# Kernel optimization log

Measured on AMD Instinct MI355X. Metric: run time of the kernel, lower is better.

The kernel has to match this reference:

```python
import jax, jax.numpy as jnp
import numpy as np

Q = 128


def _maxpool2(x):
    # 2x2 max pool, stride 2, NCHW
    return jax.lax.reduce_window(x, -jnp.inf, jax.lax.max,
                                 (1, 1, 2, 2), (1, 1, 2, 2), 'VALID')


def _conv(x, w, b):
    y = jax.lax.conv_general_dilated(x, w, window_strides=(1, 1), padding='VALID',
                                     dimension_numbers=('NCHW', 'OIHW', 'NCHW'))
    return y + b[None, :, None, None]


def setup_inputs() -> dict:
    key = jax.random.key(0)
    ks = jax.random.split(key, 16)
    B = 4096
    x = jax.random.normal(ks[0], (B, 1, 28, 28), dtype=jnp.float32)
    hash_idx1 = jax.random.randint(ks[1], (25,), 0, Q, dtype=jnp.int32)
    hash_idx2 = jax.random.randint(ks[2], (800,), 0, Q, dtype=jnp.int32)
    hash_idx3 = jax.random.randint(ks[3], (1024,), 0, Q, dtype=jnp.int32)
    # random +/-1 signs
    sgn1 = jnp.sign(jax.random.normal(ks[4], (25,), dtype=jnp.float32))
    sgn2 = jnp.sign(jax.random.normal(ks[5], (800,), dtype=jnp.float32))
    sgn3 = jnp.sign(jax.random.normal(ks[6], (1024,), dtype=jnp.float32))
    # compressed (sketched) parameters: one length-Q vector per output unit
    w1 = jax.random.normal(ks[7], (32, Q), dtype=jnp.float32) * 0.2
    b1 = jax.random.normal(ks[8], (32,), dtype=jnp.float32) * 0.05
    w2 = jax.random.normal(ks[9], (64, Q), dtype=jnp.float32) * 0.05
    b2 = jax.random.normal(ks[10], (64,), dtype=jnp.float32) * 0.05
    w3 = jax.random.normal(ks[11], (512, Q), dtype=jnp.float32) * 0.03
    b3 = jax.random.normal(ks[12], (512,), dtype=jnp.float32) * 0.05
    fc2_w = jax.random.normal(ks[13], (10, 512), dtype=jnp.float32) * 0.04
    fc2_b = jax.random.normal(ks[14], (10,), dtype=jnp.float32) * 0.05
    return {'x': x,
            'hash_idx1': hash_idx1, 'hash_idx2': hash_idx2, 'hash_idx3': hash_idx3,
            'sgn1': sgn1, 'sgn2': sgn2, 'sgn3': sgn3,
            'w1': w1, 'b1': b1, 'w2': w2, 'b2': b2, 'w3': w3, 'b3': b3,
            'fc2_w': fc2_w, 'fc2_b': fc2_b}


def reference(x, hash_idx1, hash_idx2, hash_idx3, sgn1, sgn2, sgn3,
              w1, b1, w2, b2, w3, b3, fc2_w, fc2_b):
    # SketchConv1: reconstruct dense weight via gather + sign flip
    wc1 = (w1[:, hash_idx1] * sgn1[None, :]).reshape(32, 1, 5, 5)
    h = jax.nn.relu(_maxpool2(_conv(x, wc1, b1)))          # (B,32,12,12)
    # SketchConv2
    wc2 = (w2[:, hash_idx2] * sgn2[None, :]).reshape(64, 32, 5, 5)
    h = jax.nn.relu(_maxpool2(_conv(h, wc2, b2)))          # (B,64,4,4)
    h = h.reshape(h.shape[0], -1)                          # (B,1024)
    # SketchLinear
    W3 = w3[:, hash_idx3] * sgn3[None, :]                  # (512,1024)
    h = jax.nn.relu(h @ W3.T + b3)                         # (B,512)
    logits = h @ fc2_w.T + fc2_b                           # (B,10)
    return jax.nn.log_softmax(logits, axis=1)
```

## Files before the change

### kernel.cpp

```cpp
#include <hip/hip_runtime.h>
#include <hip/hip_bf16.h>
#include <math.h>


typedef __attribute__((ext_vector_type(8))) short bf16x8;
typedef __attribute__((ext_vector_type(4))) float f32x4;

static __device__ inline ushort f2bfu(float v) {
    union { __hip_bfloat16 h; ushort u; } cv;
    cv.h = __float2bfloat16(v);
    return cv.u;
}


__global__ __launch_bounds__(256)
void k_reconstruct(const float* __restrict__ w1, const float* __restrict__ w2,
                   const float* __restrict__ w3,
                   const int* __restrict__ hi1, const int* __restrict__ hi2,
                   const int* __restrict__ hi3,
                   const float* __restrict__ s1, const float* __restrict__ s2,
                   const float* __restrict__ s3,
                   __hip_bfloat16* __restrict__ wc1f,
                   __hip_bfloat16* __restrict__ wc1s,
                   __hip_bfloat16* __restrict__ wc2f,
                   __hip_bfloat16* __restrict__ W3f) {
    const int t = blockIdx.x * blockDim.x + threadIdx.x;
    bf16x8 o;
    if (t < 256) {
        const bool shifted = t >= 128;
        const int u = t & 127;
        const int nt = u >> 6, lane = u & 63;
        const int quad = lane >> 4, l15 = lane & 15;
        const int oc = nt * 16 + l15;
        #pragma unroll
        for (int j = 0; j < 8; ++j) {
            int tt = quad * 8 + j;
            int ki = (tt * 43) >> 8;
            int kj = tt - 6 * ki;
            float v = 0.f;
            if (!shifted && ki < 5 && kj < 5) {
                int f = ki * 5 + kj;
                v = w1[oc * 128 + hi1[f]] * s1[f];
            } else if (shifted && ki < 5 && kj >= 1 && kj <= 5) {
                int f = ki * 5 + (kj - 1);
                v = w1[oc * 128 + hi1[f]] * s1[f];
            }
            o[j] = (short)f2bfu(v);
        }
        *(bf16x8*)((ushort*)(shifted ? wc1s : wc1f) + (size_t)u * 8) = o;
    } else if (t < 6656) {
        const int u = t - 256;
        const int l15 = u & 15, quad = (u >> 4) & 3;
        const int ntA = (u >> 6) & 3, tap = u >> 8;
        const int oc = ntA * 16 + l15;
        #pragma unroll
        for (int j = 0; j < 8; ++j) {
            int ic = quad * 8 + j;
            int f = ic * 25 + tap;
            o[j] = (short)f2bfu(w2[oc * 128 + hi2[f]] * s2[f]);
        }
        *(bf16x8*)((ushort*)wc2f + (size_t)u * 8) = o;
    } else if (t < 72192) {
        const int u = t - 6656;
        const int l15 = u & 15, quad = (u >> 4) & 3;
        const int kt = (u >> 6) & 31, ntile = u >> 11;
        const int n = ntile * 16 + l15;
        #pragma unroll
        for (int j = 0; j < 8; ++j) {
            int k = kt * 32 + quad * 8 + j;
            o[j] = (short)f2bfu(w3[n * 128 + hi3[k]] * s3[k]);
        }
        *(bf16x8*)((ushort*)W3f + (size_t)u * 8) = o;
    }
}

__global__ __launch_bounds__(512, 6)
void k_conv(const float* __restrict__ x,
            const __hip_bfloat16* __restrict__ wc1f,
            const __hip_bfloat16* __restrict__ wc1s,
            const __hip_bfloat16* __restrict__ wc2f,
            const float* __restrict__ b1, const float* __restrict__ b2,
            __hip_bfloat16* __restrict__ h2) {
    __shared__ __align__(16) ushort s_xb[4 * 816];
    __shared__ __align__(16) ushort s_h1[16 * 1160];

    const int tid = threadIdx.x;
    const int b0 = blockIdx.x * 4;
    const int wave = tid >> 6, lane = tid & 63;
    const int l15 = lane & 15, quad = lane >> 4;

    {
        const float4* xg = (const float4*)(x + (size_t)b0 * 784);
        for (int i = tid; i < 784; i += 512) {
            float4 v = xg[i];
            int img = i / 196;
            int pos = (i - img * 196) * 4;
            ushort* dst = &s_xb[img * 816 + pos];
            dst[0] = f2bfu(v.x); dst[1] = f2bfu(v.y);
            dst[2] = f2bfu(v.z); dst[3] = f2bfu(v.w);
        }
        if (tid < 128) {
            int img = tid >> 5, k = tid & 31;
            s_xb[img * 816 + 784 + k] = 0;
        }
    }

    bf16x8 bw1[2], bw1s[2];
    float bb1[2];
    #pragma unroll
    for (int nt = 0; nt < 2; ++nt) {
        bw1[nt]  = *(const bf16x8*)((const ushort*)wc1f + (nt * 64 + lane) * 8);
        bw1s[nt] = *(const bf16x8*)((const ushort*)wc1s + (nt * 64 + lane) * 8);
        bb1[nt] = b1[nt * 16 + l15];
    }
    __syncthreads();

    {
        const int img = wave >> 1, half = wave & 1;
        const int sub = l15 & 3;
        const ushort* srcImg = s_xb + img * 816;
        int offr[4];
        #pragma unroll
        for (int r = 0; r < 4; ++r) {
            int t = quad * 8 + 2 * r;
            int row = (t * 43) >> 8;
            int col = t - 6 * row;
            offr[r] = row * 28 + col;
        }
        const int g0 = l15 >> 3, r0 = l15 & 7;
        #pragma unroll
        for (int ii = 0; ii < 18; ++ii) {
            const int i = half * 18 + ii;
            const int pb = 4 * i + (l15 >> 2);
            const int pi = (pb * 171) >> 11;
            const int pj = pb - 12 * pi;
            const int base_e = (2 * pi + (sub >> 1)) * 28 + 2 * pj;
            const ushort* p0 = srcImg + base_e;
            union { bf16x8 v; uint u[4]; } A;
            A.u[0] = *(const uint*)(p0 + offr[0]);
            A.u[1] = *(const uint*)(p0 + offr[1]);
            A.u[2] = *(const uint*)(p0 + offr[2]);
            A.u[3] = *(const uint*)(p0 + offr[3]);
            f32x4 z = {0.f, 0.f, 0.f, 0.f};
            f32x4 ce0 = __builtin_amdgcn_mfma_f32_16x16x32_bf16(A.v, bw1[0],  z, 0, 0, 0);
            f32x4 co0 = __builtin_amdgcn_mfma_f32_16x16x32_bf16(A.v, bw1s[0], z, 0, 0, 0);
            f32x4 ce1 = __builtin_amdgcn_mfma_f32_16x16x32_bf16(A.v, bw1[1],  z, 0, 0, 0);
            f32x4 co1 = __builtin_amdgcn_mfma_f32_16x16x32_bf16(A.v, bw1s[1], z, 0, 0, 0);
            const int pbo = 4 * i + quad;
            float m0 = fmaxf(fmaxf(ce0[0], co0[1]), fmaxf(ce0[2], co0[3]));
            float m1 = fmaxf(fmaxf(ce1[0], co1[1]), fmaxf(ce1[2], co1[3]));
            s_h1[(img * 4 + g0) * 1160 + pbo * 8 + r0]     = f2bfu(fmaxf(m0 + bb1[0], 0.f));
            s_h1[(img * 4 + 2 + g0) * 1160 + pbo * 8 + r0] = f2bfu(fmaxf(m1 + bb1[1], 0.f));
        }
    }
    __syncthreads();

    const int pr = wave >> 1, nh = wave & 1;
    const int sub2 = l15 & 3;
    const int ci2 = 2 * pr + (sub2 >> 1);
    const int cj2 = 2 * (l15 >> 2) + (sub2 & 1);
    const int posBase = (ci2 * 12 + cj2) * 8;

    f32x4 acc[4][2];
    float bb2[2];
    #pragma unroll
    for (int ntl = 0; ntl < 2; ++ntl) {
        bb2[ntl] = b2[(nh * 2 + ntl) * 16 + l15];
        #pragma unroll
        for (int img = 0; img < 4; ++img)
            acc[img][ntl] = (f32x4){0.f, 0.f, 0.f, 0.f};
    }

    #pragma unroll
    for (int tap = 0; tap < 25; ++tap) {
        const int ki = tap / 5, kj = tap % 5;
        const int off = (ki * 12 + kj) * 8;
        bf16x8 a[4];
        #pragma unroll
        for (int img = 0; img < 4; ++img)
            a[img] = *(const bf16x8*)&s_h1[(img * 4 + quad) * 1160 + posBase + off];
        #pragma unroll
        for (int ntl = 0; ntl < 2; ++ntl) {
            bf16x8 bf = *(const bf16x8*)((const ushort*)wc2f +
                          ((tap * 4 + nh * 2 + ntl) * 64 + lane) * 8);
            #pragma unroll
            for (int img = 0; img < 4; ++img)
                acc[img][ntl] = __builtin_amdgcn_mfma_f32_16x16x32_bf16(
                    a[img], bf, acc[img][ntl], 0, 0, 0);
        }
    }

    #pragma unroll
    for (int img = 0; img < 4; ++img)
        #pragma unroll
        for (int ntl = 0; ntl < 2; ++ntl) {
            f32x4 c = acc[img][ntl];
            float m = fmaxf(fmaxf(c[0], c[1]), fmaxf(c[2], c[3]));
            float v = fmaxf(m + bb2[ntl], 0.f);
            h2[(size_t)(b0 + img) * 1024 + ((nh * 2 + ntl) * 16 + l15) * 16 + pr * 4 + quad] =
                __float2bfloat16(v);
        }
}

__global__ __launch_bounds__(1024)
void k_fc(const __hip_bfloat16* __restrict__ A, const __hip_bfloat16* __restrict__ W3f,
          const float* __restrict__ b3, const float* __restrict__ fc2w,
          const float* __restrict__ fc2b, float* __restrict__ out) {
    __shared__ __align__(16) ushort s_A[16 * 1032];
    __shared__ float s_h3[16 * 516];

    const int tid = threadIdx.x;
    const int wave = tid >> 6, lane = tid & 63;
    const int l15 = lane & 15, quad = lane >> 4;
    const int mBase = blockIdx.x * 16;

    {
        const uint4* g = (const uint4*)(A + (size_t)(mBase + wave) * 1024);
        uint4 v0 = g[lane * 2], v1 = g[lane * 2 + 1];
        uint4* d = (uint4*)&s_A[wave * 1032 + lane * 16];
        d[0] = v0; d[1] = v1;
    }
    __syncthreads();

    f32x4 acc[2];
    acc[0] = (f32x4){0.f, 0.f, 0.f, 0.f};
    acc[1] = (f32x4){0.f, 0.f, 0.f, 0.f};

    const ushort* aP = &s_A[l15 * 1032 + quad * 8];
    const ushort* bP0 = (const ushort*)W3f + (((size_t)(wave * 2)     * 32) * 64 + lane) * 8;
    const ushort* bP1 = (const ushort*)W3f + (((size_t)(wave * 2 + 1) * 32) * 64 + lane) * 8;
    #pragma unroll 4
    for (int kt = 0; kt < 32; ++kt) {
        bf16x8 a = *(const bf16x8*)(aP + kt * 32);
        bf16x8 bf0 = *(const bf16x8*)(bP0 + kt * 512);
        bf16x8 bf1 = *(const bf16x8*)(bP1 + kt * 512);
        acc[0] = __builtin_amdgcn_mfma_f32_16x16x32_bf16(a, bf0, acc[0], 0, 0, 0);
        acc[1] = __builtin_amdgcn_mfma_f32_16x16x32_bf16(a, bf1, acc[1], 0, 0, 0);
    }

    #pragma unroll
    for (int ntl = 0; ntl < 2; ++ntl) {
        int col = wave * 32 + ntl * 16 + l15;
        float bb = b3[col];
        #pragma unroll
        for (int r = 0; r < 4; ++r)
            s_h3[(quad * 4 + r) * 516 + col] = fmaxf(acc[ntl][r] + bb, 0.f);
    }
    __syncthreads();

    const float* hrow = &s_h3[wave * 516];
    float4 h0 = *(const float4*)&hrow[lane * 8];
    float4 h1 = *(const float4*)&hrow[lane * 8 + 4];
    float lg[10];
    #pragma unroll
    for (int c = 0; c < 10; ++c) {
        float4 w0 = *(const float4*)&fc2w[c * 512 + lane * 8];
        float4 w1 = *(const float4*)&fc2w[c * 512 + lane * 8 + 4];
        float s = h0.x * w0.x + h0.y * w0.y + h0.z * w0.z + h0.w * w0.w
                + h1.x * w1.x + h1.y * w1.y + h1.z * w1.z + h1.w * w1.w;
        s += __shfl_down(s, 32);
        s += __shfl_down(s, 16);
        s += __shfl_down(s, 8);
        s += __shfl_down(s, 4);
        s += __shfl_down(s, 2);
        s += __shfl_down(s, 1);
        lg[c] = s;
    }
    if (lane == 0) {
        float mx = -1e30f;
        #pragma unroll
        for (int c = 0; c < 10; ++c) { lg[c] += fc2b[c]; mx = fmaxf(mx, lg[c]); }
        float sum = 0.f;
        #pragma unroll
        for (int c = 0; c < 10; ++c) sum += expf(lg[c] - mx);
        float lse = mx + logf(sum);
        #pragma unroll
        for (int c = 0; c < 10; ++c)
            out[(size_t)(mBase + wave) * 10 + c] = lg[c] - lse;
    }
}

extern "C" void kernel_launch(void* const* d_in, const int* in_sizes, int n_in,
                              void* d_out, int out_size, void* d_ws, size_t ws_size,
                              hipStream_t stream) {
    const float* x    = (const float*)d_in[0];
    const int*   hi1  = (const int*)d_in[1];
    const int*   hi2  = (const int*)d_in[2];
    const int*   hi3  = (const int*)d_in[3];
    const float* s1   = (const float*)d_in[4];
    const float* s2   = (const float*)d_in[5];
    const float* s3   = (const float*)d_in[6];
    const float* w1   = (const float*)d_in[7];
    const float* b1   = (const float*)d_in[8];
    const float* w2   = (const float*)d_in[9];
    const float* b2   = (const float*)d_in[10];
    const float* w3   = (const float*)d_in[11];
    const float* b3   = (const float*)d_in[12];
    const float* fc2w = (const float*)d_in[13];
    const float* fc2b = (const float*)d_in[14];
    float* out = (float*)d_out;

    const int B = in_sizes[0] / 784;

    char* ws = (char*)d_ws;
    __hip_bfloat16* wc1f = (__hip_bfloat16*)(ws + 0);
    __hip_bfloat16* wc1s = (__hip_bfloat16*)(ws + 2048);
    __hip_bfloat16* wc2f = (__hip_bfloat16*)(ws + 4096);
    __hip_bfloat16* W3f  = (__hip_bfloat16*)(ws + 106496);
    __hip_bfloat16* h2   = (__hip_bfloat16*)(ws + 1155072);

    k_reconstruct<<<(72192 + 255) / 256, 256, 0, stream>>>(
        w1, w2, w3, hi1, hi2, hi3, s1, s2, s3, wc1f, wc1s, wc2f, W3f);
    k_conv<<<B / 4, 512, 0, stream>>>(x, wc1f, wc1s, wc2f, b1, b2, h2);
    k_fc<<<B / 16, 1024, 0, stream>>>(h2, W3f, b3, fc2w, fc2b, out);
}
```

Before: 140.4 us.

## Shrink conv blocks to two images and emit h2 in MFMA fragment layout

The conv kernel now processes 2 images per block instead of 4, halving LDS use and accumulator registers and raising the launch-bounds occupancy hint from 6 to 8 blocks. The conv output h2 is written directly in the MFMA A-fragment layout (16-row tiles interleaved by k groups), so the FC kernel can load A operands straight from global memory and skip its LDS staging and barrier. Each conv block now reuses every weight fragment across fewer images, and the conv output stores become more scattered.

```diff
diff --git a/kernel.cpp b/kernel.cpp
--- a/kernel.cpp
+++ b/kernel.cpp
@@ -74,33 +74,34 @@
     }
 }
 
-__global__ __launch_bounds__(512, 6)
+__global__ __launch_bounds__(512, 8)
 void k_conv(const float* __restrict__ x,
             const __hip_bfloat16* __restrict__ wc1f,
             const __hip_bfloat16* __restrict__ wc1s,
             const __hip_bfloat16* __restrict__ wc2f,
             const float* __restrict__ b1, const float* __restrict__ b2,
-            __hip_bfloat16* __restrict__ h2) {
-    __shared__ __align__(16) ushort s_xb[4 * 816];
-    __shared__ __align__(16) ushort s_h1[16 * 1160];
+            ushort* __restrict__ h2f) {
+    __shared__ __align__(16) ushort s_xb[2 * 816];
+    __shared__ __align__(16) ushort s_h1[8 * 1160];
 
     const int tid = threadIdx.x;
-    const int b0 = blockIdx.x * 4;
+    const int b0 = blockIdx.x * 2;
     const int wave = tid >> 6, lane = tid & 63;
     const int l15 = lane & 15, quad = lane >> 4;
 
     {
         const float4* xg = (const float4*)(x + (size_t)b0 * 784);
-        for (int i = tid; i < 784; i += 512) {
-            float4 v = xg[i];
-            int img = i / 196;
-            int pos = (i - img * 196) * 4;
+        if (tid < 392) {
+            float4 v = xg[tid];
+            int img = tid / 196;
+            int pos = (tid - img * 196) * 4;
             ushort* dst = &s_xb[img * 816 + pos];
             dst[0] = f2bfu(v.x); dst[1] = f2bfu(v.y);
             dst[2] = f2bfu(v.z); dst[3] = f2bfu(v.w);
         }
-        if (tid < 128) {
-            int img = tid >> 5, k = tid & 31;
+        if (tid >= 448 && tid < 512) {
+            int u = tid - 448;
+            int img = u >> 5, k = u & 31;
             s_xb[img * 816 + 784 + k] = 0;
         }
     }
@@ -116,7 +117,7 @@
     __syncthreads();
 
     {
-        const int img = wave >> 1, half = wave & 1;
+        const int img = wave >> 2, q = wave & 3;
         const int sub = l15 & 3;
         const ushort* srcImg = s_xb + img * 816;
         int offr[4];
@@ -129,8 +130,8 @@
         }
         const int g0 = l15 >> 3, r0 = l15 & 7;
         #pragma unroll
-        for (int ii = 0; ii < 18; ++ii) {
-            const int i = half * 18 + ii;
+        for (int ii = 0; ii < 9; ++ii) {
+            const int i = q * 9 + ii;
             const int pb = 4 * i + (l15 >> 2);
             const int pi = (pb * 171) >> 11;
             const int pj = pb - 12 * pi;
@@ -161,52 +162,50 @@
     const int cj2 = 2 * (l15 >> 2) + (sub2 & 1);
     const int posBase = (ci2 * 12 + cj2) * 8;
 
-    f32x4 acc[4][2];
+    f32x4 acc[2][2];
     float bb2[2];
     #pragma unroll
     for (int ntl = 0; ntl < 2; ++ntl) {
         bb2[ntl] = b2[(nh * 2 + ntl) * 16 + l15];
-        #pragma unroll
-        for (int img = 0; img < 4; ++img)
-            acc[img][ntl] = (f32x4){0.f, 0.f, 0.f, 0.f};
+        acc[0][ntl] = (f32x4){0.f, 0.f, 0.f, 0.f};
+        acc[1][ntl] = (f32x4){0.f, 0.f, 0.f, 0.f};
     }
 
     #pragma unroll
     for (int tap = 0; tap < 25; ++tap) {
         const int ki = tap / 5, kj = tap % 5;
         const int off = (ki * 12 + kj) * 8;
-        bf16x8 a[4];
-        #pragma unroll
-        for (int img = 0; img < 4; ++img)
-            a[img] = *(const bf16x8*)&s_h1[(img * 4 + quad) * 1160 + posBase + off];
+        bf16x8 a0 = *(const bf16x8*)&s_h1[(0 * 4 + quad) * 1160 + posBase + off];
+        bf16x8 a1 = *(const bf16x8*)&s_h1[(1 * 4 + quad) * 1160 + posBase + off];
         #pragma unroll
         for (int ntl = 0; ntl < 2; ++ntl) {
             bf16x8 bf = *(const bf16x8*)((const ushort*)wc2f +
                           ((tap * 4 + nh * 2 + ntl) * 64 + lane) * 8);
-            #pragma unroll
-            for (int img = 0; img < 4; ++img)
-                acc[img][ntl] = __builtin_amdgcn_mfma_f32_16x16x32_bf16(
-                    a[img], bf, acc[img][ntl], 0, 0, 0);
-        }
-    }
-
-    #pragma unroll
-    for (int img = 0; img < 4; ++img)
+            acc[0][ntl] = __builtin_amdgcn_mfma_f32_16x16x32_bf16(a0, bf, acc[0][ntl], 0, 0, 0);
+            acc[1][ntl] = __builtin_amdgcn_mfma_f32_16x16x32_bf16(a1, bf, acc[1][ntl], 0, 0, 0);
+        }
+    }
+
+    #pragma unroll
+    for (int img = 0; img < 2; ++img) {
+        const int img_g = b0 + img;
+        const size_t base = (size_t)(img_g >> 4) * 16384 + (img_g & 15) * 8;
         #pragma unroll
         for (int ntl = 0; ntl < 2; ++ntl) {
             f32x4 c = acc[img][ntl];
             float m = fmaxf(fmaxf(c[0], c[1]), fmaxf(c[2], c[3]));
             float v = fmaxf(m + bb2[ntl], 0.f);
-            h2[(size_t)(b0 + img) * 1024 + ((nh * 2 + ntl) * 16 + l15) * 16 + pr * 4 + quad] =
-                __float2bfloat16(v);
-        }
+            const int k = (nh * 2 + ntl) * 256 + l15 * 16 + pr * 4 + quad;
+            h2f[base + (size_t)(k >> 5) * 512 + ((k >> 3) & 3) * 128 + (k & 7)] =
+                f2bfu(v);
+        }
+    }
 }
 
 __global__ __launch_bounds__(1024)
-void k_fc(const __hip_bfloat16* __restrict__ A, const __hip_bfloat16* __restrict__ W3f,
+void k_fc(const ushort* __restrict__ h2f, const __hip_bfloat16* __restrict__ W3f,
           const float* __restrict__ b3, const float* __restrict__ fc2w,
           const float* __restrict__ fc2b, float* __restrict__ out) {
-    __shared__ __align__(16) ushort s_A[16 * 1032];
     __shared__ float s_h3[16 * 516];
 
     const int tid = threadIdx.x;
@@ -214,24 +213,16 @@
     const int l15 = lane & 15, quad = lane >> 4;
     const int mBase = blockIdx.x * 16;
 
-    {
-        const uint4* g = (const uint4*)(A + (size_t)(mBase + wave) * 1024);
-        uint4 v0 = g[lane * 2], v1 = g[lane * 2 + 1];
-        uint4* d = (uint4*)&s_A[wave * 1032 + lane * 16];
-        d[0] = v0; d[1] = v1;
-    }
-    __syncthreads();
-
     f32x4 acc[2];
     acc[0] = (f32x4){0.f, 0.f, 0.f, 0.f};
     acc[1] = (f32x4){0.f, 0.f, 0.f, 0.f};
 
-    const ushort* aP = &s_A[l15 * 1032 + quad * 8];
+    const ushort* aP  = h2f + (size_t)blockIdx.x * 16384 + lane * 8;
     const ushort* bP0 = (const ushort*)W3f + (((size_t)(wave * 2)     * 32) * 64 + lane) * 8;
     const ushort* bP1 = (const ushort*)W3f + (((size_t)(wave * 2 + 1) * 32) * 64 + lane) * 8;
     #pragma unroll 4
     for (int kt = 0; kt < 32; ++kt) {
-        bf16x8 a = *(const bf16x8*)(aP + kt * 32);
+        bf16x8 a   = *(const bf16x8*)(aP + kt * 512);
         bf16x8 bf0 = *(const bf16x8*)(bP0 + kt * 512);
         bf16x8 bf1 = *(const bf16x8*)(bP1 + kt * 512);
         acc[0] = __builtin_amdgcn_mfma_f32_16x16x32_bf16(a, bf0, acc[0], 0, 0, 0);
@@ -307,10 +298,10 @@
     __hip_bfloat16* wc1s = (__hip_bfloat16*)(ws + 2048);
     __hip_bfloat16* wc2f = (__hip_bfloat16*)(ws + 4096);
     __hip_bfloat16* W3f  = (__hip_bfloat16*)(ws + 106496);
-    __hip_bfloat16* h2   = (__hip_bfloat16*)(ws + 1155072);
+    ushort*         h2f  = (ushort*)(ws + 1155072);
 
     k_reconstruct<<<(72192 + 255) / 256, 256, 0, stream>>>(
         w1, w2, w3, hi1, hi2, hi3, s1, s2, s3, wc1f, wc1s, wc2f, W3f);
-    k_conv<<<B / 4, 512, 0, stream>>>(x, wc1f, wc1s, wc2f, b1, b2, h2);
-    k_fc<<<B / 16, 1024, 0, stream>>>(h2, W3f, b3, fc2w, fc2b, out);
-}
+    k_conv<<<B / 2, 512, 0, stream>>>(x, wc1f, wc1s, wc2f, b1, b2, h2f);
+    k_fc<<<B / 16, 1024, 0, stream>>>(h2f, W3f, b3, fc2w, fc2b, out);
+}
```

Result: slower. 149.2 us (+6.3%).

## Store conv output in MFMA fragment layout and drop LDS staging in FC

Applied to the files above, without the earlier changes.

The conv kernel now writes its pooled activations straight into an MFMA A-fragment order: per 16-image group, one 512-element block per k-tile. This lets the FC kernel load A fragments directly from global memory with contiguous 16-byte loads, with no shared-memory staging or barrier. The FC kernel is also reshaped to 512 threads, with each wave computing four 16-column N tiles instead of two and handling two rows in the log-softmax epilogue. The conv stores become scattered 2-byte writes, and each FC block still runs only 8 waves over 256 blocks.

```diff
diff --git a/kernel.cpp b/kernel.cpp
--- a/kernel.cpp
+++ b/kernel.cpp
@@ -80,7 +80,7 @@
             const __hip_bfloat16* __restrict__ wc1s,
             const __hip_bfloat16* __restrict__ wc2f,
             const float* __restrict__ b1, const float* __restrict__ b2,
-            __hip_bfloat16* __restrict__ h2) {
+            ushort* __restrict__ h2f) {
     __shared__ __align__(16) ushort s_xb[4 * 816];
     __shared__ __align__(16) ushort s_h1[16 * 1160];
 
@@ -191,22 +191,25 @@
     }
 
     #pragma unroll
-    for (int img = 0; img < 4; ++img)
+    for (int img = 0; img < 4; ++img) {
+        const int img_g = b0 + img;
+        const size_t base = (size_t)(img_g >> 4) * 16384 + (img_g & 15) * 8;
         #pragma unroll
         for (int ntl = 0; ntl < 2; ++ntl) {
             f32x4 c = acc[img][ntl];
             float m = fmaxf(fmaxf(c[0], c[1]), fmaxf(c[2], c[3]));
             float v = fmaxf(m + bb2[ntl], 0.f);
-            h2[(size_t)(b0 + img) * 1024 + ((nh * 2 + ntl) * 16 + l15) * 16 + pr * 4 + quad] =
-                __float2bfloat16(v);
-        }
-}
-
-__global__ __launch_bounds__(1024)
-void k_fc(const __hip_bfloat16* __restrict__ A, const __hip_bfloat16* __restrict__ W3f,
+            const int k = (nh * 2 + ntl) * 256 + l15 * 16 + pr * 4 + quad;
+            h2f[base + (size_t)(k >> 5) * 512 + ((k >> 3) & 3) * 128 + (k & 7)] =
+                f2bfu(v);
+        }
+    }
+}
+
+__global__ __launch_bounds__(512, 4)
+void k_fc(const ushort* __restrict__ h2f, const __hip_bfloat16* __restrict__ W3f,
           const float* __restrict__ b3, const float* __restrict__ fc2w,
           const float* __restrict__ fc2b, float* __restrict__ out) {
-    __shared__ __align__(16) ushort s_A[16 * 1032];
     __shared__ float s_h3[16 * 516];
 
     const int tid = threadIdx.x;
@@ -214,33 +217,29 @@
     const int l15 = lane & 15, quad = lane >> 4;
     const int mBase = blockIdx.x * 16;
 
-    {
-        const uint4* g = (const uint4*)(A + (size_t)(mBase + wave) * 1024);
-        uint4 v0 = g[lane * 2], v1 = g[lane * 2 + 1];
-        uint4* d = (uint4*)&s_A[wave * 1032 + lane * 16];
-        d[0] = v0; d[1] = v1;
-    }
-    __syncthreads();
-
-    f32x4 acc[2];
-    acc[0] = (f32x4){0.f, 0.f, 0.f, 0.f};
-    acc[1] = (f32x4){0.f, 0.f, 0.f, 0.f};
-
-    const ushort* aP = &s_A[l15 * 1032 + quad * 8];
-    const ushort* bP0 = (const ushort*)W3f + (((size_t)(wave * 2)     * 32) * 64 + lane) * 8;
-    const ushort* bP1 = (const ushort*)W3f + (((size_t)(wave * 2 + 1) * 32) * 64 + lane) * 8;
-    #pragma unroll 4
+    f32x4 acc[4];
+    #pragma unroll
+    for (int ntl = 0; ntl < 4; ++ntl) acc[ntl] = (f32x4){0.f, 0.f, 0.f, 0.f};
+
+    const ushort* aP = h2f + (size_t)blockIdx.x * 16384 + lane * 8;
+    const ushort* bP[4];
+    #pragma unroll
+    for (int ntl = 0; ntl < 4; ++ntl)
+        bP[ntl] = (const ushort*)W3f + ((size_t)(wave * 4 + ntl) * 2048 + lane) * 8;
+
+    #pragma unroll 2
     for (int kt = 0; kt < 32; ++kt) {
-        bf16x8 a = *(const bf16x8*)(aP + kt * 32);
-        bf16x8 bf0 = *(const bf16x8*)(bP0 + kt * 512);
-        bf16x8 bf1 = *(const bf16x8*)(bP1 + kt * 512);
-        acc[0] = __builtin_amdgcn_mfma_f32_16x16x32_bf16(a, bf0, acc[0], 0, 0, 0);
-        acc[1] = __builtin_amdgcn_mfma_f32_16x16x32_bf16(a, bf1, acc[1], 0, 0, 0);
-    }
-
-    #pragma unroll
-    for (int ntl = 0; ntl < 2; ++ntl) {
-        int col = wave * 32 + ntl * 16 + l15;
+        bf16x8 a = *(const bf16x8*)(aP + kt * 512);
+        #pragma unroll
+        for (int ntl = 0; ntl < 4; ++ntl) {
+            bf16x8 bf = *(const bf16x8*)(bP[ntl] + kt * 512);
+            acc[ntl] = __builtin_amdgcn_mfma_f32_16x16x32_bf16(a, bf, acc[ntl], 0, 0, 0);
+        }
+    }
+
+    #pragma unroll
+    for (int ntl = 0; ntl < 4; ++ntl) {
+        int col = wave * 64 + ntl * 16 + l15;
         float bb = b3[col];
         #pragma unroll
         for (int r = 0; r < 4; ++r)
@@ -248,35 +247,39 @@
     }
     __syncthreads();
 
-    const float* hrow = &s_h3[wave * 516];
-    float4 h0 = *(const float4*)&hrow[lane * 8];
-    float4 h1 = *(const float4*)&hrow[lane * 8 + 4];
-    float lg[10];
-    #pragma unroll
-    for (int c = 0; c < 10; ++c) {
-        float4 w0 = *(const float4*)&fc2w[c * 512 + lane * 8];
-        float4 w1 = *(const float4*)&fc2w[c * 512 + lane * 8 + 4];
-        float s = h0.x * w0.x + h0.y * w0.y + h0.z * w0.z + h0.w * w0.w
-                + h1.x * w1.x + h1.y * w1.y + h1.z * w1.z + h1.w * w1.w;
-        s += __shfl_down(s, 32);
-        s += __shfl_down(s, 16);
-        s += __shfl_down(s, 8);
-        s += __shfl_down(s, 4);
-        s += __shfl_down(s, 2);
-        s += __shfl_down(s, 1);
-        lg[c] = s;
-    }
-    if (lane == 0) {
-        float mx = -1e30f;
-        #pragma unroll
-        for (int c = 0; c < 10; ++c) { lg[c] += fc2b[c]; mx = fmaxf(mx, lg[c]); }
-        float sum = 0.f;
-        #pragma unroll
-        for (int c = 0; c < 10; ++c) sum += expf(lg[c] - mx);
-        float lse = mx + logf(sum);
-        #pragma unroll
-        for (int c = 0; c < 10; ++c)
-            out[(size_t)(mBase + wave) * 10 + c] = lg[c] - lse;
+    #pragma unroll
+    for (int i2 = 0; i2 < 2; ++i2) {
+        const int m = wave * 2 + i2;
+        const float* hrow = &s_h3[m * 516];
+        float4 h0 = *(const float4*)&hrow[lane * 8];
+        float4 h1 = *(const float4*)&hrow[lane * 8 + 4];
+        float lg[10];
+        #pragma unroll
+        for (int c = 0; c < 10; ++c) {
+            float4 w0 = *(const float4*)&fc2w[c * 512 + lane * 8];
+            float4 w1 = *(const float4*)&fc2w[c * 512 + lane * 8 + 4];
+            float s = h0.x * w0.x + h0.y * w0.y + h0.z * w0.z + h0.w * w0.w
+                    + h1.x * w1.x + h1.y * w1.y + h1.z * w1.z + h1.w * w1.w;
+            s += __shfl_down(s, 32);
+            s += __shfl_down(s, 16);
+            s += __shfl_down(s, 8);
+            s += __shfl_down(s, 4);
+            s += __shfl_down(s, 2);
+            s += __shfl_down(s, 1);
+            lg[c] = s;
+        }
+        if (lane == 0) {
+            float mx = -1e30f;
+            #pragma unroll
+            for (int c = 0; c < 10; ++c) { lg[c] += fc2b[c]; mx = fmaxf(mx, lg[c]); }
+            float sum = 0.f;
+            #pragma unroll
+            for (int c = 0; c < 10; ++c) sum += expf(lg[c] - mx);
+            float lse = mx + logf(sum);
+            #pragma unroll
+            for (int c = 0; c < 10; ++c)
+                out[(size_t)(mBase + m) * 10 + c] = lg[c] - lse;
+        }
     }
 }
 
@@ -307,10 +310,10 @@
     __hip_bfloat16* wc1s = (__hip_bfloat16*)(ws + 2048);
     __hip_bfloat16* wc2f = (__hip_bfloat16*)(ws + 4096);
     __hip_bfloat16* W3f  = (__hip_bfloat16*)(ws + 106496);
-    __hip_bfloat16* h2   = (__hip_bfloat16*)(ws + 1155072);
+    ushort*         h2f  = (ushort*)(ws + 1155072);
 
     k_reconstruct<<<(72192 + 255) / 256, 256, 0, stream>>>(
         w1, w2, w3, hi1, hi2, hi3, s1, s2, s3, wc1f, wc1s, wc2f, W3f);
-    k_conv<<<B / 4, 512, 0, stream>>>(x, wc1f, wc1s, wc2f, b1, b2, h2);
-    k_fc<<<B / 16, 1024, 0, stream>>>(h2, W3f, b3, fc2w, fc2b, out);
-}
+    k_conv<<<B / 4, 512, 0, stream>>>(x, wc1f, wc1s, wc2f, b1, b2, h2f);
+    k_fc<<<B / 16, 512, 0, stream>>>(h2f, W3f, b3, fc2w, fc2b, out);
+}
```

New measurement: 146.2 us. 1.04x slower.

## Pad conv1 input rows and store h2 in MFMA fragment layout

Applied to the files above, without the earlier changes.

The staged conv1 input in shared memory now uses a row stride of 30 instead of 28, which changes which banks the unaligned 32-bit A-operand loads hit. The conv kernel writes its h2 activations directly in the MFMA A-fragment order that the FC kernel consumes, so the FC kernel loads a contiguous 32 KB block with coalesced vector copies and reads fragments with a simple lane*8 stride. The cost is scattered 2-byte global stores from the conv kernel and a batch layout tied to groups of 16 images.

```diff
diff --git a/kernel.cpp b/kernel.cpp
--- a/kernel.cpp
+++ b/kernel.cpp
@@ -80,8 +80,8 @@
             const __hip_bfloat16* __restrict__ wc1s,
             const __hip_bfloat16* __restrict__ wc2f,
             const float* __restrict__ b1, const float* __restrict__ b2,
-            __hip_bfloat16* __restrict__ h2) {
-    __shared__ __align__(16) ushort s_xb[4 * 816];
+            ushort* __restrict__ h2f) {
+    __shared__ __align__(16) ushort s_xb[4 * 880];
     __shared__ __align__(16) ushort s_h1[16 * 1160];
 
     const int tid = threadIdx.x;
@@ -95,13 +95,14 @@
             float4 v = xg[i];
             int img = i / 196;
             int pos = (i - img * 196) * 4;
-            ushort* dst = &s_xb[img * 816 + pos];
+            int row = pos / 28, col = pos - row * 28;
+            ushort* dst = &s_xb[img * 880 + row * 30 + col];
             dst[0] = f2bfu(v.x); dst[1] = f2bfu(v.y);
             dst[2] = f2bfu(v.z); dst[3] = f2bfu(v.w);
         }
-        if (tid < 128) {
-            int img = tid >> 5, k = tid & 31;
-            s_xb[img * 816 + 784 + k] = 0;
+        if (tid < 160) {
+            int img = tid / 40, k = tid - 40 * (tid / 40);
+            s_xb[img * 880 + 840 + k] = 0;
         }
     }
 
@@ -118,14 +119,14 @@
     {
         const int img = wave >> 1, half = wave & 1;
         const int sub = l15 & 3;
-        const ushort* srcImg = s_xb + img * 816;
+        const ushort* srcImg = s_xb + img * 880;
         int offr[4];
         #pragma unroll
         for (int r = 0; r < 4; ++r) {
             int t = quad * 8 + 2 * r;
             int row = (t * 43) >> 8;
             int col = t - 6 * row;
-            offr[r] = row * 28 + col;
+            offr[r] = row * 30 + col;
         }
         const int g0 = l15 >> 3, r0 = l15 & 7;
         #pragma unroll
@@ -134,7 +135,7 @@
             const int pb = 4 * i + (l15 >> 2);
             const int pi = (pb * 171) >> 11;
             const int pj = pb - 12 * pi;
-            const int base_e = (2 * pi + (sub >> 1)) * 28 + 2 * pj;
+            const int base_e = (2 * pi + (sub >> 1)) * 30 + 2 * pj;
             const ushort* p0 = srcImg + base_e;
             union { bf16x8 v; uint u[4]; } A;
             A.u[0] = *(const uint*)(p0 + offr[0]);
@@ -191,22 +192,26 @@
     }
 
     #pragma unroll
-    for (int img = 0; img < 4; ++img)
+    for (int img = 0; img < 4; ++img) {
+        const int img_g = b0 + img;
+        const size_t base = (size_t)(img_g >> 4) * 16384 + (img_g & 15) * 8;
         #pragma unroll
         for (int ntl = 0; ntl < 2; ++ntl) {
             f32x4 c = acc[img][ntl];
             float m = fmaxf(fmaxf(c[0], c[1]), fmaxf(c[2], c[3]));
             float v = fmaxf(m + bb2[ntl], 0.f);
-            h2[(size_t)(b0 + img) * 1024 + ((nh * 2 + ntl) * 16 + l15) * 16 + pr * 4 + quad] =
-                __float2bfloat16(v);
-        }
+            const int k = (nh * 2 + ntl) * 256 + l15 * 16 + pr * 4 + quad;
+            h2f[base + (size_t)(k >> 5) * 512 + ((k >> 3) & 3) * 128 + (k & 7)] =
+                f2bfu(v);
+        }
+    }
 }
 
 __global__ __launch_bounds__(1024)
-void k_fc(const __hip_bfloat16* __restrict__ A, const __hip_bfloat16* __restrict__ W3f,
+void k_fc(const ushort* __restrict__ h2f, const __hip_bfloat16* __restrict__ W3f,
           const float* __restrict__ b3, const float* __restrict__ fc2w,
           const float* __restrict__ fc2b, float* __restrict__ out) {
-    __shared__ __align__(16) ushort s_A[16 * 1032];
+    __shared__ __align__(16) ushort s_A[16384];
     __shared__ float s_h3[16 * 516];
 
     const int tid = threadIdx.x;
@@ -215,10 +220,10 @@
     const int mBase = blockIdx.x * 16;
 
     {
-        const uint4* g = (const uint4*)(A + (size_t)(mBase + wave) * 1024);
-        uint4 v0 = g[lane * 2], v1 = g[lane * 2 + 1];
-        uint4* d = (uint4*)&s_A[wave * 1032 + lane * 16];
-        d[0] = v0; d[1] = v1;
+        const uint4* g = (const uint4*)(h2f + (size_t)blockIdx.x * 16384);
+        uint4* d = (uint4*)s_A;
+        d[tid] = g[tid];
+        d[tid + 1024] = g[tid + 1024];
     }
     __syncthreads();
 
@@ -226,12 +231,12 @@
     acc[0] = (f32x4){0.f, 0.f, 0.f, 0.f};
     acc[1] = (f32x4){0.f, 0.f, 0.f, 0.f};
 
-    const ushort* aP = &s_A[l15 * 1032 + quad * 8];
-    const ushort* bP0 = (const ushort*)W3f + (((size_t)(wave * 2)     * 32) * 64 + lane) * 8;
-    const ushort* bP1 = (const ushort*)W3f + (((size_t)(wave * 2 + 1) * 32) * 64 + lane) * 8;
+    const ushort* aP  = s_A + lane * 8;
+    const ushort* bP0 = (const ushort*)W3f + ((size_t)(wave * 2)     * 16384 + lane * 8);
+    const ushort* bP1 = (const ushort*)W3f + ((size_t)(wave * 2 + 1) * 16384 + lane * 8);
     #pragma unroll 4
     for (int kt = 0; kt < 32; ++kt) {
-        bf16x8 a = *(const bf16x8*)(aP + kt * 32);
+        bf16x8 a   = *(const bf16x8*)(aP + kt * 512);
         bf16x8 bf0 = *(const bf16x8*)(bP0 + kt * 512);
         bf16x8 bf1 = *(const bf16x8*)(bP1 + kt * 512);
         acc[0] = __builtin_amdgcn_mfma_f32_16x16x32_bf16(a, bf0, acc[0], 0, 0, 0);
@@ -307,10 +312,10 @@
     __hip_bfloat16* wc1s = (__hip_bfloat16*)(ws + 2048);
     __hip_bfloat16* wc2f = (__hip_bfloat16*)(ws + 4096);
     __hip_bfloat16* W3f  = (__hip_bfloat16*)(ws + 106496);
-    __hip_bfloat16* h2   = (__hip_bfloat16*)(ws + 1155072);
+    ushort*         h2f  = (ushort*)(ws + 1155072);
 
     k_reconstruct<<<(72192 + 255) / 256, 256, 0, stream>>>(
         w1, w2, w3, hi1, hi2, hi3, s1, s2, s3, wc1f, wc1s, wc2f, W3f);
-    k_conv<<<B / 4, 512, 0, stream>>>(x, wc1f, wc1s, wc2f, b1, b2, h2);
-    k_fc<<<B / 16, 1024, 0, stream>>>(h2, W3f, b3, fc2w, fc2b, out);
-}
+    k_conv<<<B / 4, 512, 0, stream>>>(x, wc1f, wc1s, wc2f, b1, b2, h2f);
+    k_fc<<<B / 16, 1024, 0, stream>>>(h2f, W3f, b3, fc2w, fc2b, out);
+}
```

Result: no change. 142.0 us (+1.2%).
